# Optimization experiments

Measured on AMD Instinct MI355X. Metric: run time of the kernel, lower is better.

The kernel has to match this reference:

```python
import jax, jax.numpy as jnp
import numpy as np

N = 1024      # total ROIs packed across the ragged batch
S = 14        # roi_output_size
C = 256       # conv_dim == feature_size
NC = 80       # num_classes
K = 4         # num_convs
DN = ('NHWC', 'HWIO', 'NHWC')


def setup_inputs() -> dict:
    key = jax.random.key(0)
    ks = jax.random.split(key, 5)
    x = jax.random.normal(ks[0], (N, S, S, C), jnp.float32)
    # 4 identical-shape 3x3 convs (C->C), stacked on a leading axis
    Wc = jax.random.normal(ks[1], (K, 3, 3, C, C), jnp.float32) * 0.03
    bc = jnp.zeros((K, C), jnp.float32)
    # 2x2 stride-2 transpose conv (C->C)
    Wt = jax.random.normal(ks[2], (2, 2, C, C), jnp.float32) * 0.03
    bt = jnp.zeros((C,), jnp.float32)
    # 1x1 mask predictor (C->NC), no activation
    Wm = jax.random.normal(ks[3], (1, 1, C, NC), jnp.float32) * 0.03
    bm = jnp.zeros((NC,), jnp.float32)
    return {"x": x, "Wc": Wc, "bc": bc, "Wt": Wt, "bt": bt, "Wm": Wm, "bm": bm}


def reference(x, Wc, bc, Wt, bt, Wm, bm):
    # Packed-batch equivalent of the nested tf.map_fn: conv math is
    # independent per ROI, so one batched conv over all ROIs is identical.
    for i in range(K):  # fixed small layer count
        x = jax.lax.conv_general_dilated(x, Wc[i], (1, 1), 'SAME', dimension_numbers=DN)
        x = jax.nn.relu(x + bc[i])
    # Conv2DTranspose(kernel=2, stride=2, padding='valid'), relu
    x = jax.lax.conv_transpose(x, Wt, (2, 2), 'VALID', dimension_numbers=DN)
    x = jax.nn.relu(x + bt)
    # 1x1 conv, linear activation -> [N, 28, 28, NC]
    x = jax.lax.conv_general_dilated(x, Wm, (1, 1), 'SAME', dimension_numbers=DN) + bm
    return x
```

## Files before the change

kernel.cpp:

```cpp
#include <hip/hip_runtime.h>


typedef _Float16 f16x8 __attribute__((ext_vector_type(8)));
typedef float    f32x4 __attribute__((ext_vector_type(4)));
typedef unsigned short u16;
typedef unsigned int   u32;

__device__ __forceinline__ u16 f2h(float f) {
  union { _Float16 h; u16 u; } c; c.h = (_Float16)f; return c.u;
}

__device__ __forceinline__ void store8(u16* dst, const u16* o) {
  uint4 v;
  v.x = (u32)o[0] | ((u32)o[1] << 16);
  v.y = (u32)o[2] | ((u32)o[3] << 16);
  v.z = (u32)o[4] | ((u32)o[5] << 16);
  v.w = (u32)o[6] | ((u32)o[7] << 16);
  *(uint4*)dst = v;
}

__global__ void prep_weights(const float* __restrict__ Wc, const float* __restrict__ Wt,
                             const float* __restrict__ Wm,
                             u16* __restrict__ WbP, u16* __restrict__ WtP,
                             u16* __restrict__ WmP) {
  int id = blockIdx.x * 256 + threadIdx.x;
  u16 o[8];
  if (id < 294912) {
    int li = id & 63; int rest = id >> 6;
    int ct = rest & 15; rest >>= 4;
    int kc = rest & 7;  rest >>= 3;
    int co  = ct * 16 + (li & 15);
    int ci0 = kc * 32 + (li >> 4) * 8;
#pragma unroll
    for (int j = 0; j < 8; j++) o[j] = f2h(Wc[(rest * 256 + ci0 + j) * 256 + co]);
    store8(&WbP[id * 8], o);
  } else if (id < 327680) {
    int id2 = id - 294912;
    int li = id2 & 63; int rest = id2 >> 6;
    int ct = rest & 15; rest >>= 4;
    int kc = rest & 7;  rest >>= 3;
    int srcq = 3 - rest;
    int co  = ct * 16 + (li & 15);
    int ci0 = kc * 32 + (li >> 4) * 8;
#pragma unroll
    for (int j = 0; j < 8; j++) o[j] = f2h(Wt[(srcq * 256 + ci0 + j) * 256 + co]);
    store8(&WtP[id2 * 8], o);
  } else if (id < 330240) {
    int id3 = id - 327680;
    int li = id3 & 63; int rest = id3 >> 6;
    int kc = rest / 5, nt = rest % 5;
    int nc  = nt * 16 + (li & 15);
    int ci0 = kc * 32 + (li >> 4) * 8;
#pragma unroll
    for (int j = 0; j < 8; j++) o[j] = f2h(Wm[(ci0 + j) * 80 + nc]);
    store8(&WmP[id3 * 8], o);
  }
}

template <bool INF32>
__global__ __launch_bounds__(256, 2)
void conv_layer(const void* __restrict__ in_, const u16* __restrict__ WbP,
                const float* __restrict__ bc, u16* __restrict__ out, int layer) {
  __shared__ u16 sA[126 * 136 + 128];
  const int ZP = 126 * 136;
  const int tid = threadIdx.x;
  const int w = tid >> 6, lane = tid & 63, q = lane >> 4, r = lane & 15;
  const int roi = blockIdx.x, mhalf = blockIdx.y;
  const int mbase = mhalf * 112;
  const int base_px = mhalf ? 98 : 0;
  const int n_px   = mhalf ? 98 : 126;
  const int rot = (blockIdx.x + mhalf) % 9;
  if (tid < 64) ((u32*)(sA + ZP))[tid] = 0u;

  int py[7], px[7];
#pragma unroll
  for (int mt = 0; mt < 7; mt++) {
    int p = mbase + mt * 16 + r;
    py[mt] = (p < 196) ? (p / 14) : 1000;
    px[mt] = p % 14;
  }
  f32x4 acc[7][4];
#pragma unroll
  for (int mt = 0; mt < 7; mt++)
#pragma unroll
    for (int nf = 0; nf < 4; nf++) acc[mt][nf] = (f32x4){0.f, 0.f, 0.f, 0.f};

  const float* xin = (const float*)in_;
  const u16*   yin = (const u16*)in_;

  const u16* wb = WbP + (size_t)layer * 589824 + (w * 4) * 512 + lane * 8;

  f16x8 b0[4], b1[4];
#pragma unroll
  for (int nf = 0; nf < 4; nf++)
    b0[nf] = *(const f16x8*)&wb[rot * 65536 + nf * 512];

  for (int kh = 0; kh < 2; kh++) {
    if (kh) __syncthreads();
    if (INF32) {
      for (int c = tid; c < n_px * 32; c += 256) {
        int pix = c >> 5, c4 = (c & 31) * 4;
        const float4 v = *(const float4*)&xin[((size_t)roi * 196 + base_px + pix) * 256 + kh * 128 + c4];
        ushort4 h; h.x = f2h(v.x); h.y = f2h(v.y); h.z = f2h(v.z); h.w = f2h(v.w);
        *(ushort4*)&sA[pix * 136 + c4] = h;
      }
    } else {
      for (int c = tid; c < n_px * 16; c += 256) {
        int pix = c >> 4, c8 = (c & 15) * 8;
        *(uint4*)&sA[pix * 136 + c8] =
            *(const uint4*)&yin[((size_t)roi * 196 + base_px + pix) * 256 + kh * 128 + c8];
      }
    }
    __syncthreads();

    for (int t = 0; t < 9; t++) {
      int tap = t + rot; if (tap >= 9) tap -= 9;
      const int dy = tap / 3 - 1, dx = tap % 3 - 1;
      int offs[7];
#pragma unroll
      for (int mt = 0; mt < 7; mt++) {
        int ny = py[mt] + dy, nx = px[mt] + dx;
        bool v = ((u32)ny < 14u) && ((u32)nx < 14u);
        offs[mt] = v ? ((ny * 14 + nx) - base_px) * 136 : ZP;
      }
#pragma unroll
      for (int kk = 0; kk < 4; kk++) {
        int nt = t, nh = kh, nk = kk + 1;
        if (kk == 3) {
          nk = 0; nt = t + 1;
          if (nt == 9) {
            if (kh == 0) { nt = 0; nh = 1; }
            else         { nt = 8; nh = 1; nk = 3; }
          }
        }
        int ntap = nt + rot; if (ntap >= 9) ntap -= 9;
        const u16* wn = wb + (ntap * 8 + nh * 4 + nk) * 8192;
        if ((kk & 1) == 0) {
#pragma unroll
          for (int nf = 0; nf < 4; nf++) b1[nf] = *(const f16x8*)&wn[nf * 512];
#pragma unroll
          for (int mt = 0; mt < 7; mt++) {
            f16x8 a = *(const f16x8*)&sA[offs[mt] + kk * 32 + q * 8];
#pragma unroll
            for (int nf = 0; nf < 4; nf++)
              acc[mt][nf] = __builtin_amdgcn_mfma_f32_16x16x32_f16(a, b0[nf], acc[mt][nf], 0, 0, 0);
          }
        } else {
#pragma unroll
          for (int nf = 0; nf < 4; nf++) b0[nf] = *(const f16x8*)&wn[nf * 512];
#pragma unroll
          for (int mt = 0; mt < 7; mt++) {
            f16x8 a = *(const f16x8*)&sA[offs[mt] + kk * 32 + q * 8];
#pragma unroll
            for (int nf = 0; nf < 4; nf++)
              acc[mt][nf] = __builtin_amdgcn_mfma_f32_16x16x32_f16(a, b1[nf], acc[mt][nf], 0, 0, 0);
          }
        }
      }
    }
  }

  float bias[4];
#pragma unroll
  for (int nf = 0; nf < 4; nf++) bias[nf] = bc[layer * 256 + (w * 4 + nf) * 16 + r];
#pragma unroll
  for (int mt = 0; mt < 7; mt++) {
#pragma unroll
    for (int jj = 0; jj < 4; jj++) {
      int p = mbase + mt * 16 + q * 4 + jj;
      if (p < 196) {
#pragma unroll
        for (int nf = 0; nf < 4; nf++) {
          float v = acc[mt][nf][jj] + bias[nf];
          v = fmaxf(v, 0.f);
          out[((size_t)roi * 196 + p) * 256 + (w * 4 + nf) * 16 + r] = f2h(v);
        }
      }
    }
  }
}

__global__ __launch_bounds__(256, 2)
void tail_fused(const u16* __restrict__ y4, const u16* __restrict__ WtP,
                const u16* __restrict__ WmP, const float* __restrict__ bt,
                const float* __restrict__ bm, float* __restrict__ out) {
  __shared__ u16 sA[112 * 264 + 128];
  const int ZP = 112 * 264;
  const int tid = threadIdx.x;
  const int w = tid >> 6, lane = tid & 63, q = lane >> 4, r = lane & 15;
  const int roi = blockIdx.x, ab = blockIdx.y, mbase = blockIdx.z * 112;
  const int n_px = mbase ? 84 : 112;
  if (tid < 64) ((u32*)(sA + ZP))[tid] = 0u;

  int offs[7];
#pragma unroll
  for (int mt = 0; mt < 7; mt++) {
    int p = mbase + mt * 16 + r;
    offs[mt] = (p < 196) ? (mt * 16 + r) * 136 : ZP;
  }
  f32x4 acc[7][4];
#pragma unroll
  for (int mt = 0; mt < 7; mt++)
#pragma unroll
    for (int nf = 0; nf < 4; nf++) acc[mt][nf] = (f32x4){0.f, 0.f, 0.f, 0.f};

  const u16* wt = WtP + ab * 65536 + (w * 4) * 512 + lane * 8;
  f16x8 b0[4], b1[4];
#pragma unroll
  for (int nf = 0; nf < 4; nf++) b0[nf] = *(const f16x8*)&wt[nf * 512];

  for (int kh = 0; kh < 2; kh++) {
    if (kh) __syncthreads();
    for (int c = tid; c < n_px * 16; c += 256) {
      int pix = c >> 4, c8 = (c & 15) * 8;
      *(uint4*)&sA[pix * 136 + c8] =
          *(const uint4*)&y4[((size_t)roi * 196 + mbase + pix) * 256 + kh * 128 + c8];
    }
    __syncthreads();
#pragma unroll
    for (int kk = 0; kk < 4; kk++) {
      int nc_ = kh * 4 + kk + 1; if (nc_ > 7) nc_ = 7;
      const u16* wn = wt + nc_ * 8192;
      if ((kk & 1) == 0) {
#pragma unroll
        for (int nf = 0; nf < 4; nf++) b1[nf] = *(const f16x8*)&wn[nf * 512];
#pragma unroll
        for (int mt = 0; mt < 7; mt++) {
          f16x8 a = *(const f16x8*)&sA[offs[mt] + kk * 32 + q * 8];
#pragma unroll
          for (int nf = 0; nf < 4; nf++)
            acc[mt][nf] = __builtin_amdgcn_mfma_f32_16x16x32_f16(a, b0[nf], acc[mt][nf], 0, 0, 0);
        }
      } else {
#pragma unroll
        for (int nf = 0; nf < 4; nf++) b0[nf] = *(const f16x8*)&wn[nf * 512];
#pragma unroll
        for (int mt = 0; mt < 7; mt++) {
          f16x8 a = *(const f16x8*)&sA[offs[mt] + kk * 32 + q * 8];
#pragma unroll
          for (int nf = 0; nf < 4; nf++)
            acc[mt][nf] = __builtin_amdgcn_mfma_f32_16x16x32_f16(a, b1[nf], acc[mt][nf], 0, 0, 0);
        }
      }
    }
  }

  __syncthreads();
  float btv[4];
#pragma unroll
  for (int nf = 0; nf < 4; nf++) btv[nf] = bt[(w * 4 + nf) * 16 + r];
#pragma unroll
  for (int mt = 0; mt < 7; mt++) {
#pragma unroll
    for (int jj = 0; jj < 4; jj++) {
      int row = mt * 16 + q * 4 + jj;
#pragma unroll
      for (int nf = 0; nf < 4; nf++) {
        float v = fmaxf(acc[mt][nf][jj] + btv[nf], 0.f);
        sA[row * 264 + (w * 4 + nf) * 16 + r] = f2h(v);
      }
    }
  }
  __syncthreads();

  float bmv[5];
#pragma unroll
  for (int nt = 0; nt < 5; nt++) bmv[nt] = bm[nt * 16 + r];
  const int a_ = ab >> 1, b_ = ab & 1;
  for (int tt = w; tt < 7; tt += 4) {
    f32x4 a2[5];
#pragma unroll
    for (int nt = 0; nt < 5; nt++) a2[nt] = (f32x4){0.f, 0.f, 0.f, 0.f};
#pragma unroll
    for (int kc = 0; kc < 8; kc++) {
      f16x8 af = *(const f16x8*)&sA[(tt * 16 + r) * 264 + kc * 32 + q * 8];
#pragma unroll
      for (int nt = 0; nt < 5; nt++) {
        f16x8 bw = *(const f16x8*)&WmP[((kc * 5 + nt) * 64 + lane) * 8];
        a2[nt] = __builtin_amdgcn_mfma_f32_16x16x32_f16(af, bw, a2[nt], 0, 0, 0);
      }
    }
#pragma unroll
    for (int jj = 0; jj < 4; jj++) {
      int row = tt * 16 + q * 4 + jj;
      int p = mbase + row;
      if (p < 196) {
        int y = p / 14, x = p % 14;
        size_t base = (size_t)roi * 62720 + (2 * y + a_) * 2240 + (2 * x + b_) * 80;
#pragma unroll
        for (int nt = 0; nt < 5; nt++) out[base + nt * 16 + r] = a2[nt][jj] + bmv[nt];
      }
    }
  }
}

extern "C" void kernel_launch(void* const* d_in, const int* in_sizes, int n_in,
                              void* d_out, int out_size, void* d_ws, size_t ws_size,
                              hipStream_t stream) {
  const float* x  = (const float*)d_in[0];
  const float* Wc = (const float*)d_in[1];
  const float* bc = (const float*)d_in[2];
  const float* Wt = (const float*)d_in[3];
  const float* bt = (const float*)d_in[4];
  const float* Wm = (const float*)d_in[5];
  const float* bm = (const float*)d_in[6];
  float* out = (float*)d_out;

  char* ws = (char*)d_ws;
  u16* WbP = (u16*)(ws);
  u16* WtP = (u16*)(ws + 4718592);
  u16* WmP = (u16*)(ws + 5242880);
  u16* yA  = (u16*)(ws + 6291456);
  u16* yB  = (u16*)(ws + 6291456 + 102760448);

  prep_weights<<<1290, 256, 0, stream>>>(Wc, Wt, Wm, WbP, WtP, WmP);

  dim3 cg(1024, 2);
  conv_layer<true ><<<cg, 256, 0, stream>>>(x,  WbP, bc, yA, 0);
  conv_layer<false><<<cg, 256, 0, stream>>>(yA, WbP, bc, yB, 1);
  conv_layer<false><<<cg, 256, 0, stream>>>(yB, WbP, bc, yA, 2);
  conv_layer<false><<<cg, 256, 0, stream>>>(yA, WbP, bc, yB, 3);

  tail_fused<<<dim3(1024, 4, 2), 256, 0, stream>>>(yB, WtP, WmP, bt, bm, out);
}
```

Before: 1.433 ms.

## Double-buffer channel halves in LDS with register prefetch of second half

For the fp16 conv layers and the fused tail, the second 128-channel half of each ROI's input is loaded into registers right after the first half is staged, so the global loads overlap the first half's MFMA work. The data is then written to a second LDS buffer, which removes one barrier before the second half. The cost is a doubled LDS footprint (about 68KB for conv and 61KB for the tail) and up to 8 extra uint4 registers per thread. Both could lower occupancy below the 2 blocks per CU that launch_bounds requests, and the added register pressure may cause spills.

```diff
diff --git a/kernel.cpp b/kernel.cpp
--- a/kernel.cpp
+++ b/kernel.cpp
@@ -61,8 +61,9 @@
 __global__ __launch_bounds__(256, 2)
 void conv_layer(const void* __restrict__ in_, const u16* __restrict__ WbP,
                 const float* __restrict__ bc, u16* __restrict__ out, int layer) {
-  __shared__ u16 sA[126 * 136 + 128];
-  const int ZP = 126 * 136;
+  __shared__ u16 sA[2 * 17136 + 128];
+  const int BUF = 17136;
+  const int ZPI = 2 * 17136;
   const int tid = threadIdx.x;
   const int w = tid >> 6, lane = tid & 63, q = lane >> 4, r = lane & 15;
   const int roi = blockIdx.x, mhalf = blockIdx.y;
@@ -70,7 +71,7 @@
   const int base_px = mhalf ? 98 : 0;
   const int n_px   = mhalf ? 98 : 126;
   const int rot = (blockIdx.x + mhalf) % 9;
-  if (tid < 64) ((u32*)(sA + ZP))[tid] = 0u;
+  if (tid < 64) ((u32*)(sA + ZPI))[tid] = 0u;
 
   int py[7], px[7];
 #pragma unroll
@@ -85,8 +86,8 @@
 #pragma unroll
     for (int nf = 0; nf < 4; nf++) acc[mt][nf] = (f32x4){0.f, 0.f, 0.f, 0.f};
 
-  const float* xin = (const float*)in_;
-  const u16*   yin = (const u16*)in_;
+  const float* xrow = (const float*)in_ + ((size_t)blockIdx.x * 196 + base_px) * 256;
+  const u16*   yrow = (const u16*)in_   + ((size_t)blockIdx.x * 196 + base_px) * 256;
 
   const u16* wb = WbP + (size_t)layer * 589824 + (w * 4) * 512 + lane * 8;
 
@@ -95,23 +96,60 @@
   for (int nf = 0; nf < 4; nf++)
     b0[nf] = *(const f16x8*)&wb[rot * 65536 + nf * 512];
 
+  if (INF32) {
+    for (int c = tid; c < n_px * 32; c += 256) {
+      int pix = c >> 5, c4 = (c & 31) * 4;
+      const float4 v = *(const float4*)&xrow[pix * 256 + c4];
+      ushort4 h; h.x = f2h(v.x); h.y = f2h(v.y); h.z = f2h(v.z); h.w = f2h(v.w);
+      *(ushort4*)&sA[pix * 136 + c4] = h;
+    }
+  } else {
+#pragma unroll
+    for (int i = 0; i < 8; i++) {
+      int c = tid + i * 256;
+      if (c < n_px * 16) {
+        int pix = c >> 4, c8 = (c & 15) * 8;
+        *(uint4*)&sA[pix * 136 + c8] = *(const uint4*)&yrow[pix * 256 + c8];
+      }
+    }
+  }
+  __syncthreads();
+
+  uint4 pre[8];
+  if (!INF32) {
+#pragma unroll
+    for (int i = 0; i < 8; i++) {
+      int c = tid + i * 256;
+      if (c < n_px * 16) {
+        int pix = c >> 4, c8 = (c & 15) * 8;
+        pre[i] = *(const uint4*)&yrow[pix * 256 + 128 + c8];
+      }
+    }
+  }
+
   for (int kh = 0; kh < 2; kh++) {
-    if (kh) __syncthreads();
-    if (INF32) {
-      for (int c = tid; c < n_px * 32; c += 256) {
-        int pix = c >> 5, c4 = (c & 31) * 4;
-        const float4 v = *(const float4*)&xin[((size_t)roi * 196 + base_px + pix) * 256 + kh * 128 + c4];
-        ushort4 h; h.x = f2h(v.x); h.y = f2h(v.y); h.z = f2h(v.z); h.w = f2h(v.w);
-        *(ushort4*)&sA[pix * 136 + c4] = h;
-      }
-    } else {
-      for (int c = tid; c < n_px * 16; c += 256) {
-        int pix = c >> 4, c8 = (c & 15) * 8;
-        *(uint4*)&sA[pix * 136 + c8] =
-            *(const uint4*)&yin[((size_t)roi * 196 + base_px + pix) * 256 + kh * 128 + c8];
-      }
-    }
-    __syncthreads();
+    if (kh) {
+      if (INF32) {
+        __syncthreads();
+        for (int c = tid; c < n_px * 32; c += 256) {
+          int pix = c >> 5, c4 = (c & 31) * 4;
+          const float4 v = *(const float4*)&xrow[pix * 256 + 128 + c4];
+          ushort4 h; h.x = f2h(v.x); h.y = f2h(v.y); h.z = f2h(v.z); h.w = f2h(v.w);
+          *(ushort4*)&sA[pix * 136 + c4] = h;
+        }
+      } else {
+#pragma unroll
+        for (int i = 0; i < 8; i++) {
+          int c = tid + i * 256;
+          if (c < n_px * 16) {
+            int pix = c >> 4, c8 = (c & 15) * 8;
+            *(uint4*)&sA[BUF + pix * 136 + c8] = pre[i];
+          }
+        }
+      }
+      __syncthreads();
+    }
+    const int bufb = INF32 ? 0 : kh * BUF;
 
     for (int t = 0; t < 9; t++) {
       int tap = t + rot; if (tap >= 9) tap -= 9;
@@ -121,7 +159,7 @@
       for (int mt = 0; mt < 7; mt++) {
         int ny = py[mt] + dy, nx = px[mt] + dx;
         bool v = ((u32)ny < 14u) && ((u32)nx < 14u);
-        offs[mt] = v ? ((ny * 14 + nx) - base_px) * 136 : ZP;
+        offs[mt] = v ? (bufb + ((ny * 14 + nx) - base_px) * 136) : ZPI;
       }
 #pragma unroll
       for (int kk = 0; kk < 4; kk++) {
@@ -173,50 +211,79 @@
         for (int nf = 0; nf < 4; nf++) {
           float v = acc[mt][nf][jj] + bias[nf];
           v = fmaxf(v, 0.f);
-          out[((size_t)roi * 196 + p) * 256 + (w * 4 + nf) * 16 + r] = f2h(v);
-        }
-      }
-    }
-  }
+          out[((size_t)blockIdx.x * 196 + p) * 256 + (w * 4 + nf) * 16 + r] = f2h(v);
+        }
+      }
+    }
+  }
+  (void)roi;
 }
 
 __global__ __launch_bounds__(256, 2)
 void tail_fused(const u16* __restrict__ y4, const u16* __restrict__ WtP,
                 const u16* __restrict__ WmP, const float* __restrict__ bt,
                 const float* __restrict__ bm, float* __restrict__ out) {
-  __shared__ u16 sA[112 * 264 + 128];
-  const int ZP = 112 * 264;
+  __shared__ u16 sA[2 * 15232 + 128];
+  const int BUF = 15232;
+  const int ZPI = 2 * 15232;
   const int tid = threadIdx.x;
   const int w = tid >> 6, lane = tid & 63, q = lane >> 4, r = lane & 15;
   const int roi = blockIdx.x, ab = blockIdx.y, mbase = blockIdx.z * 112;
   const int n_px = mbase ? 84 : 112;
-  if (tid < 64) ((u32*)(sA + ZP))[tid] = 0u;
-
-  int offs[7];
+  if (tid < 64) ((u32*)(sA + ZPI))[tid] = 0u;
+
+  int roffs[7];
 #pragma unroll
   for (int mt = 0; mt < 7; mt++) {
     int p = mbase + mt * 16 + r;
-    offs[mt] = (p < 196) ? (mt * 16 + r) * 136 : ZP;
+    roffs[mt] = (p < 196) ? (mt * 16 + r) * 136 : -1;
   }
   f32x4 acc[7][4];
 #pragma unroll
   for (int mt = 0; mt < 7; mt++)
 #pragma unroll
     for (int nf = 0; nf < 4; nf++) acc[mt][nf] = (f32x4){0.f, 0.f, 0.f, 0.f};
+
+  const u16* yrow = y4 + ((size_t)roi * 196 + mbase) * 256;
 
   const u16* wt = WtP + ab * 65536 + (w * 4) * 512 + lane * 8;
   f16x8 b0[4], b1[4];
 #pragma unroll
   for (int nf = 0; nf < 4; nf++) b0[nf] = *(const f16x8*)&wt[nf * 512];
 
+#pragma unroll
+  for (int i = 0; i < 7; i++) {
+    int c = tid + i * 256;
+    if (c < n_px * 16) {
+      int pix = c >> 4, c8 = (c & 15) * 8;
+      *(uint4*)&sA[pix * 136 + c8] = *(const uint4*)&yrow[pix * 256 + c8];
+    }
+  }
+  __syncthreads();
+
+  uint4 pre[7];
+#pragma unroll
+  for (int i = 0; i < 7; i++) {
+    int c = tid + i * 256;
+    if (c < n_px * 16) {
+      int pix = c >> 4, c8 = (c & 15) * 8;
+      pre[i] = *(const uint4*)&yrow[pix * 256 + 128 + c8];
+    }
+  }
+
   for (int kh = 0; kh < 2; kh++) {
-    if (kh) __syncthreads();
-    for (int c = tid; c < n_px * 16; c += 256) {
-      int pix = c >> 4, c8 = (c & 15) * 8;
-      *(uint4*)&sA[pix * 136 + c8] =
-          *(const uint4*)&y4[((size_t)roi * 196 + mbase + pix) * 256 + kh * 128 + c8];
-    }
-    __syncthreads();
+    if (kh) {
+#pragma unroll
+      for (int i = 0; i < 7; i++) {
+        int c = tid + i * 256;
+        if (c < n_px * 16) {
+          int pix = c >> 4, c8 = (c & 15) * 8;
+          *(uint4*)&sA[BUF + pix * 136 + c8] = pre[i];
+        }
+      }
+      __syncthreads();
+    }
+    const int bufb = kh * BUF;
 #pragma unroll
     for (int kk = 0; kk < 4; kk++) {
       int nc_ = kh * 4 + kk + 1; if (nc_ > 7) nc_ = 7;
@@ -226,7 +293,8 @@
         for (int nf = 0; nf < 4; nf++) b1[nf] = *(const f16x8*)&wn[nf * 512];
 #pragma unroll
         for (int mt = 0; mt < 7; mt++) {
-          f16x8 a = *(const f16x8*)&sA[offs[mt] + kk * 32 + q * 8];
+          int o = (roffs[mt] < 0) ? ZPI : (bufb + roffs[mt]);
+          f16x8 a = *(const f16x8*)&sA[o + kk * 32 + q * 8];
 #pragma unroll
           for (int nf = 0; nf < 4; nf++)
             acc[mt][nf] = __builtin_amdgcn_mfma_f32_16x16x32_f16(a, b0[nf], acc[mt][nf], 0, 0, 0);
@@ -236,7 +304,8 @@
         for (int nf = 0; nf < 4; nf++) b0[nf] = *(const f16x8*)&wn[nf * 512];
 #pragma unroll
         for (int mt = 0; mt < 7; mt++) {
-          f16x8 a = *(const f16x8*)&sA[offs[mt] + kk * 32 + q * 8];
+          int o = (roffs[mt] < 0) ? ZPI : (bufb + roffs[mt]);
+          f16x8 a = *(const f16x8*)&sA[o + kk * 32 + q * 8];
 #pragma unroll
           for (int nf = 0; nf < 4; nf++)
             acc[mt][nf] = __builtin_amdgcn_mfma_f32_16x16x32_f16(a, b1[nf], acc[mt][nf], 0, 0, 0);
```

New measurement: 1.566 ms. 9.3% more time.

## Split conv output channels across blocks and XOR-swizzle shared tile

Applied to the files above, without the earlier changes.

Layers 1-3 of the 3x3 conv now split the 256 output channels across two blocks per ROI half, so each wave holds two 16-channel accumulator tiles instead of four. This frees registers, so launch bounds ask for three blocks per SM. The shared input tile drops its 136-element padded stride for a 128-element stride with an XOR swizzle of 8-element chunks, meant to avoid LDS bank conflicts while saving shared memory. The trade-off is that each ROI's input tile is loaded and converted twice, doubling activation reads from global memory for those layers.

```diff
diff --git a/kernel.cpp b/kernel.cpp
--- a/kernel.cpp
+++ b/kernel.cpp
@@ -57,19 +57,21 @@
   }
 }
 
-template <bool INF32>
-__global__ __launch_bounds__(256, 2)
+template <bool INF32, int NF>
+__global__ __launch_bounds__(256, NF == 2 ? 3 : 2)
 void conv_layer(const void* __restrict__ in_, const u16* __restrict__ WbP,
                 const float* __restrict__ bc, u16* __restrict__ out, int layer) {
-  __shared__ u16 sA[126 * 136 + 128];
-  const int ZP = 126 * 136;
+  __shared__ u16 sA[126 * 128 + 128];
+  const int ZP = 126 * 128;
   const int tid = threadIdx.x;
   const int w = tid >> 6, lane = tid & 63, q = lane >> 4, r = lane & 15;
-  const int roi = blockIdx.x, mhalf = blockIdx.y;
+  const int CS = 4 / NF;
+  const int roi = blockIdx.x / CS, cs = blockIdx.x % CS;
+  const int mhalf = blockIdx.y;
   const int mbase = mhalf * 112;
   const int base_px = mhalf ? 98 : 0;
   const int n_px   = mhalf ? 98 : 126;
-  const int rot = (blockIdx.x + mhalf) % 9;
+  const int rot = (roi + mhalf) % 9;
   if (tid < 64) ((u32*)(sA + ZP))[tid] = 0u;
 
   int py[7], px[7];
@@ -79,36 +81,38 @@
     py[mt] = (p < 196) ? (p / 14) : 1000;
     px[mt] = p % 14;
   }
-  f32x4 acc[7][4];
+  f32x4 acc[7][NF];
 #pragma unroll
   for (int mt = 0; mt < 7; mt++)
 #pragma unroll
-    for (int nf = 0; nf < 4; nf++) acc[mt][nf] = (f32x4){0.f, 0.f, 0.f, 0.f};
-
-  const float* xin = (const float*)in_;
-  const u16*   yin = (const u16*)in_;
-
-  const u16* wb = WbP + (size_t)layer * 589824 + (w * 4) * 512 + lane * 8;
-
-  f16x8 b0[4], b1[4];
-#pragma unroll
-  for (int nf = 0; nf < 4; nf++)
+    for (int nf = 0; nf < NF; nf++) acc[mt][nf] = (f32x4){0.f, 0.f, 0.f, 0.f};
+
+  const float* xrow = (const float*)in_ + ((size_t)roi * 196 + base_px) * 256;
+  const u16*   yrow = (const u16*)in_   + ((size_t)roi * 196 + base_px) * 256;
+
+  const int ct0 = cs * (4 * NF) + w * NF;
+  const u16* wb = WbP + (size_t)layer * 589824 + ct0 * 512 + lane * 8;
+
+  f16x8 b0[NF], b1[NF];
+#pragma unroll
+  for (int nf = 0; nf < NF; nf++)
     b0[nf] = *(const f16x8*)&wb[rot * 65536 + nf * 512];
 
   for (int kh = 0; kh < 2; kh++) {
     if (kh) __syncthreads();
     if (INF32) {
       for (int c = tid; c < n_px * 32; c += 256) {
-        int pix = c >> 5, c4 = (c & 31) * 4;
-        const float4 v = *(const float4*)&xin[((size_t)roi * 196 + base_px + pix) * 256 + kh * 128 + c4];
+        int pix = c >> 5, cc = c & 31;
+        const float4 v = *(const float4*)&xrow[pix * 256 + kh * 128 + cc * 4];
         ushort4 h; h.x = f2h(v.x); h.y = f2h(v.y); h.z = f2h(v.z); h.w = f2h(v.w);
-        *(ushort4*)&sA[pix * 136 + c4] = h;
+        int e = pix * 128 + (((cc >> 1) ^ (pix & 15)) << 3) + ((cc & 1) << 2);
+        *(ushort4*)&sA[e] = h;
       }
     } else {
       for (int c = tid; c < n_px * 16; c += 256) {
-        int pix = c >> 4, c8 = (c & 15) * 8;
-        *(uint4*)&sA[pix * 136 + c8] =
-            *(const uint4*)&yin[((size_t)roi * 196 + base_px + pix) * 256 + kh * 128 + c8];
+        int pix = c >> 4, ch = c & 15;
+        int e = pix * 128 + ((ch ^ (pix & 15)) << 3);
+        *(uint4*)&sA[e] = *(const uint4*)&yrow[pix * 256 + kh * 128 + ch * 8];
       }
     }
     __syncthreads();
@@ -116,12 +120,14 @@
     for (int t = 0; t < 9; t++) {
       int tap = t + rot; if (tap >= 9) tap -= 9;
       const int dy = tap / 3 - 1, dx = tap % 3 - 1;
-      int offs[7];
+      int base_e[7], sw8[7];
 #pragma unroll
       for (int mt = 0; mt < 7; mt++) {
         int ny = py[mt] + dy, nx = px[mt] + dx;
         bool v = ((u32)ny < 14u) && ((u32)nx < 14u);
-        offs[mt] = v ? ((ny * 14 + nx) - base_px) * 136 : ZP;
+        int pixg = (ny * 14 + nx) - base_px;
+        base_e[mt] = v ? pixg * 128 : ZP;
+        sw8[mt]    = v ? ((pixg & 15) << 3) : 0;
       }
 #pragma unroll
       for (int kk = 0; kk < 4; kk++) {
@@ -135,24 +141,25 @@
         }
         int ntap = nt + rot; if (ntap >= 9) ntap -= 9;
         const u16* wn = wb + (ntap * 8 + nh * 4 + nk) * 8192;
+        const int ck8 = kk * 32 + q * 8;
         if ((kk & 1) == 0) {
 #pragma unroll
-          for (int nf = 0; nf < 4; nf++) b1[nf] = *(const f16x8*)&wn[nf * 512];
+          for (int nf = 0; nf < NF; nf++) b1[nf] = *(const f16x8*)&wn[nf * 512];
 #pragma unroll
           for (int mt = 0; mt < 7; mt++) {
-            f16x8 a = *(const f16x8*)&sA[offs[mt] + kk * 32 + q * 8];
-#pragma unroll
-            for (int nf = 0; nf < 4; nf++)
+            f16x8 a = *(const f16x8*)&sA[base_e[mt] + (ck8 ^ sw8[mt])];
+#pragma unroll
+            for (int nf = 0; nf < NF; nf++)
               acc[mt][nf] = __builtin_amdgcn_mfma_f32_16x16x32_f16(a, b0[nf], acc[mt][nf], 0, 0, 0);
           }
         } else {
 #pragma unroll
-          for (int nf = 0; nf < 4; nf++) b0[nf] = *(const f16x8*)&wn[nf * 512];
+          for (int nf = 0; nf < NF; nf++) b0[nf] = *(const f16x8*)&wn[nf * 512];
 #pragma unroll
           for (int mt = 0; mt < 7; mt++) {
-            f16x8 a = *(const f16x8*)&sA[offs[mt] + kk * 32 + q * 8];
-#pragma unroll
-            for (int nf = 0; nf < 4; nf++)
+            f16x8 a = *(const f16x8*)&sA[base_e[mt] + (ck8 ^ sw8[mt])];
+#pragma unroll
+            for (int nf = 0; nf < NF; nf++)
               acc[mt][nf] = __builtin_amdgcn_mfma_f32_16x16x32_f16(a, b1[nf], acc[mt][nf], 0, 0, 0);
           }
         }
@@ -160,9 +167,9 @@
     }
   }
 
-  float bias[4];
-#pragma unroll
-  for (int nf = 0; nf < 4; nf++) bias[nf] = bc[layer * 256 + (w * 4 + nf) * 16 + r];
+  float bias[NF];
+#pragma unroll
+  for (int nf = 0; nf < NF; nf++) bias[nf] = bc[layer * 256 + (ct0 + nf) * 16 + r];
 #pragma unroll
   for (int mt = 0; mt < 7; mt++) {
 #pragma unroll
@@ -170,10 +177,10 @@
       int p = mbase + mt * 16 + q * 4 + jj;
       if (p < 196) {
 #pragma unroll
-        for (int nf = 0; nf < 4; nf++) {
+        for (int nf = 0; nf < NF; nf++) {
           float v = acc[mt][nf][jj] + bias[nf];
           v = fmaxf(v, 0.f);
-          out[((size_t)roi * 196 + p) * 256 + (w * 4 + nf) * 16 + r] = f2h(v);
+          out[((size_t)roi * 196 + p) * 256 + (ct0 + nf) * 16 + r] = f2h(v);
         }
       }
     }
@@ -315,11 +322,10 @@
 
   prep_weights<<<1290, 256, 0, stream>>>(Wc, Wt, Wm, WbP, WtP, WmP);
 
-  dim3 cg(1024, 2);
-  conv_layer<true ><<<cg, 256, 0, stream>>>(x,  WbP, bc, yA, 0);
-  conv_layer<false><<<cg, 256, 0, stream>>>(yA, WbP, bc, yB, 1);
-  conv_layer<false><<<cg, 256, 0, stream>>>(yB, WbP, bc, yA, 2);
-  conv_layer<false><<<cg, 256, 0, stream>>>(yA, WbP, bc, yB, 3);
+  conv_layer<true , 4><<<dim3(1024, 2), 256, 0, stream>>>(x,  WbP, bc, yA, 0);
+  conv_layer<false, 2><<<dim3(2048, 2), 256, 0, stream>>>(yA, WbP, bc, yB, 1);
+  conv_layer<false, 2><<<dim3(2048, 2), 256, 0, stream>>>(yB, WbP, bc, yA, 2);
+  conv_layer<false, 2><<<dim3(2048, 2), 256, 0, stream>>>(yA, WbP, bc, yB, 3);
 
   tail_fused<<<dim3(1024, 4, 2), 256, 0, stream>>>(yB, WtP, WmP, bt, bm, out);
 }
```

New measurement: 1.499 ms. 1.05x slower.
